# Kernel optimization log

Measured on AMD Instinct MI355X. Metric: run time of the kernel, lower is better.

## Reference

```python
import jax, jax.numpy as jnp
import numpy as np

D_MODEL = 512
D_FF = 4 * D_MODEL
NUM_EXPERTS = 8
TOP_K = 2
NUM_TASKS = 16
D_TASK = 64
BATCH = 8
SEQ = 4096
LN_EPS = 1e-5


def setup_inputs() -> dict:
    key = jax.random.key(0)
    ks = jax.random.split(key, 10)
    s_in = 1.0 / np.sqrt(D_MODEL)
    s_ff = 1.0 / np.sqrt(D_FF)
    s_g = 1.0 / np.sqrt(D_MODEL + D_TASK)
    return {
        "x": jax.random.normal(ks[0], (BATCH, SEQ, D_MODEL), jnp.float32),
        "task_id": jax.random.randint(ks[1], (BATCH,), 0, NUM_TASKS),
        "w1": jax.random.normal(ks[2], (NUM_EXPERTS, D_MODEL, D_FF), jnp.float32) * s_in,
        "b1": jnp.zeros((NUM_EXPERTS, D_FF), jnp.float32),
        "w2": jax.random.normal(ks[3], (NUM_EXPERTS, D_FF, D_MODEL), jnp.float32) * s_ff,
        "b2": jnp.zeros((NUM_EXPERTS, D_MODEL), jnp.float32),
        "task_emb": jax.random.normal(ks[4], (NUM_TASKS, D_TASK), jnp.float32),
        "gate_w": jax.random.normal(ks[5], (D_MODEL + D_TASK, NUM_EXPERTS), jnp.float32) * s_g,
        "gate_b": jnp.zeros((NUM_EXPERTS,), jnp.float32),
    }


def reference(x, task_id, w1, b1, w2, b2, task_emb, gate_w, gate_b):
    B, S, D = x.shape
    E = w1.shape[0]

    # F.layer_norm(x, x.shape[1:]): normalize over (seq, d_model) jointly, no affine
    mean = jnp.mean(x, axis=(1, 2), keepdims=True)
    var = jnp.var(x, axis=(1, 2), keepdims=True)
    x_norm = (x - mean) * jax.lax.rsqrt(var + LN_EPS)

    t_emb = task_emb[task_id]                       # [B, d_task]
    t_emb = jnp.broadcast_to(t_emb[:, None, :], (B, S, t_emb.shape[-1]))
    gate_in = jnp.concatenate([x_norm, t_emb], axis=-1)
    logits = gate_in @ gate_w + gate_b              # [B, S, E]

    topk_logits, topk_idx = jax.lax.top_k(logits, TOP_K)   # [B, S, K]
    topk_probs = jax.nn.softmax(topk_logits, axis=-1)

    flat_x = x.reshape(-1, D)                       # [T, D]
    flat_idx = topk_idx.reshape(-1, TOP_K)          # [T, K]
    flat_p = topk_probs.reshape(-1, TOP_K)          # [T, K]

    assign = jax.nn.one_hot(flat_idx, E, dtype=x.dtype)    # [T, K, E]
    combine = jnp.einsum("tk,tke->te", flat_p, assign)     # [T, E] per-token expert weight

    out = jnp.zeros_like(flat_x)
    for e in range(E):  # fixed small expert loop
        h = jax.nn.silu(flat_x @ w1[e] + b1[e])
        y = h @ w2[e] + b2[e]
        out = out + y * combine[:, e:e + 1]
    final_output = out.reshape(B, S, D)

    usage = jnp.sum(assign, axis=(0, 1))            # [E] assignment counts
    usage_mean = jnp.mean(usage) + 1e-6
    usage_std = jnp.std(usage, ddof=1)              # torch.std is unbiased
    lb_loss = (usage_std / usage_mean) ** 2

    return final_output, lb_loss, topk_idx, task_id
```

## Files before the change

### kernel.cpp

```cpp
#include <hip/hip_runtime.h>

#define NB      8
#define SEQ     4096
#define DM      512
#define DFF     2048
#define NE      8
#define NTOK    32768
#define NPB     2097152
#define MAXROWS 66560
#define MAXTILES 520

#define OUT_LB   16777216
#define OUT_TOPK 16777217
#define OUT_TASK 16842753

#define WS_BSTATS   0
#define WS_DMEAN    8192
#define WS_DRSTD    8256
#define WS_DCOLSUM  8320
#define WS_DTASK    8384
#define WS_HIST     8896
#define WS_CURSOR   8928
#define WS_SEGOFF   8960
#define WS_HDR_END  9216
#define WS_ROUTE_E  9216
#define WS_ROUTE_P  271360
#define WS_ATOK     533504
#define WS_APROB    799744
#define WS_TOKPOS   1065984
#define WS_RAW      1328128
#define WS_W1T      3425280
#define WS_W2T      20202496
#define WS_XB       36979712
#define WS_Y        70534144
#define WS_H        138691584

typedef __attribute__((ext_vector_type(4))) float  f32x4;
typedef __attribute__((ext_vector_type(8))) __bf16 bf16x8;
typedef __attribute__((ext_vector_type(8))) short  s16x8;

__device__ __forceinline__ unsigned short f2bf(float f) {
    unsigned int u = __builtin_bit_cast(unsigned int, f);
    u += 0x7FFFu + ((u >> 16) & 1u);
    return (unsigned short)(u >> 16);
}
__device__ __forceinline__ float bf2f(unsigned short b) {
    unsigned int u = ((unsigned int)b) << 16;
    return __builtin_bit_cast(float, u);
}
__device__ __forceinline__ unsigned int pkbf(float a, float b) {
    unsigned int r;
    asm("v_cvt_pk_bf16_f32 %0, %1, %2" : "=v"(r) : "v"(a), "v"(b));
    return r;
}
__device__ __forceinline__ float silu_f(float v) {
    return v * __builtin_amdgcn_rcpf(1.0f + __expf(-v));
}

#define GLDS16(g, l)                                                              \
    __builtin_amdgcn_global_load_lds(                                             \
        (const __attribute__((address_space(1))) unsigned int*)(const void*)(g),  \
        (__attribute__((address_space(3))) unsigned int*)(void*)(l), 16, 0, 0)

__global__ void k_transpose_bf16(const float* __restrict__ in,
                                 unsigned short* __restrict__ outT,
                                 int R, int C) {
    __shared__ float tile[32][33];
    int e = blockIdx.z;
    const float* src = in + (size_t)e * R * C;
    unsigned short* dst = outT + (size_t)e * R * C;
    int tx = threadIdx.x & 31, ty = threadIdx.x >> 5;
    int c0 = blockIdx.x * 32, r0 = blockIdx.y * 32;
#pragma unroll
    for (int i = 0; i < 4; i++) {
        int r = r0 + ty + i * 8;
        tile[ty + i * 8][tx] = src[(size_t)r * C + c0 + tx];
    }
    __syncthreads();
#pragma unroll
    for (int i = 0; i < 4; i++) {
        int rr = c0 + ty + i * 8;
        dst[(size_t)rr * R + r0 + tx] = f2bf(tile[tx][ty + i * 8]);
    }
}

#define GQPAD 1032
__global__ void __launch_bounds__(256) k_xgate(const float* __restrict__ x,
                                               const float* __restrict__ gw,
                                               unsigned short* __restrict__ xb,
                                               double* __restrict__ bstats,
                                               double* __restrict__ raw) {
    __shared__ float gws[4 * GQPAD];
    int t = threadIdx.x;
#pragma unroll
    for (int i = 0; i < 16; i++) {
        int idx = i * 256 + t;
        int row = idx >> 3, e = idx & 7;
        gws[(row >> 7) * GQPAD + (row & 127) * 8 + e] = gw[idx];
    }
    __syncthreads();

    int token = blockIdx.x * 64 + (t >> 2);
    int q = t & 3;
    const float4* xp = (const float4*)(x + (size_t)token * DM + q * 128);
    unsigned short* xbp = xb + (size_t)token * DM + q * 128;
    const float* gq = &gws[q * GQPAD];

    double acc[8] = {0, 0, 0, 0, 0, 0, 0, 0};
    double s = 0.0, ss = 0.0;
#pragma unroll 4
    for (int i = 0; i < 32; i += 2) {
        float4 v0 = xp[i];
        float4 v1 = xp[i + 1];
        {
            double dx = v0.x, dy = v0.y, dz = v0.z, dw = v0.w;
            const float* g = &gq[i * 32];
#pragma unroll
            for (int e = 0; e < 8; e++)
                acc[e] += dx * (double)g[e] + dy * (double)g[8 + e]
                        + dz * (double)g[16 + e] + dw * (double)g[24 + e];
            s  += dx + dy + dz + dw;
            ss += dx * dx + dy * dy + dz * dz + dw * dw;
        }
        {
            double dx = v1.x, dy = v1.y, dz = v1.z, dw = v1.w;
            const float* g = &gq[(i + 1) * 32];
#pragma unroll
            for (int e = 0; e < 8; e++)
                acc[e] += dx * (double)g[e] + dy * (double)g[8 + e]
                        + dz * (double)g[16 + e] + dw * (double)g[24 + e];
            s  += dx + dy + dz + dw;
            ss += dx * dx + dy * dy + dz * dz + dw * dw;
        }
        s16x8 o = {(short)f2bf(v0.x), (short)f2bf(v0.y), (short)f2bf(v0.z), (short)f2bf(v0.w),
                   (short)f2bf(v1.x), (short)f2bf(v1.y), (short)f2bf(v1.z), (short)f2bf(v1.w)};
        *(s16x8*)(xbp + i * 4) = o;
    }

#pragma unroll
    for (int e = 0; e < 8; e++) {
        acc[e] += __shfl_xor(acc[e], 1);
        acc[e] += __shfl_xor(acc[e], 2);
    }
    if (q == 0) {
#pragma unroll
        for (int e = 0; e < 8; e++) raw[(size_t)token * 8 + e] = acc[e];
    }

    for (int o = 32; o; o >>= 1) { s += __shfl_down(s, o); ss += __shfl_down(ss, o); }
    __shared__ double as_[4], ass_[4];
    int w = t >> 6;
    if ((t & 63) == 0) { as_[w] = s; ass_[w] = ss; }
    __syncthreads();
    if (t == 0) {
        s  = as_[0] + as_[1] + as_[2] + as_[3];
        ss = ass_[0] + ass_[1] + ass_[2] + ass_[3];
        bstats[blockIdx.x * 2]     = s;
        bstats[blockIdx.x * 2 + 1] = ss;
    }
}

__global__ void k_finalize(const double* __restrict__ bstats,
                           double* __restrict__ dmean, double* __restrict__ drstd,
                           double* __restrict__ dcolsum, double* __restrict__ dtask,
                           const float* __restrict__ gw, const float* __restrict__ gb,
                           const float* __restrict__ temb, const int* __restrict__ task_id,
                           float* __restrict__ out_task) {
    int t = threadIdx.x;
    if (t < 8) {
        double s = 0.0, ss = 0.0;
        for (int i = 0; i < 64; i++) {
            s  += bstats[(t * 64 + i) * 2];
            ss += bstats[(t * 64 + i) * 2 + 1];
        }
        double N = (double)NPB;
        double m = s / N;
        double var = ss / N - m * m;
        dmean[t] = m;
        drstd[t] = 1.0 / sqrt(var + 1e-5);
    }
    __shared__ double colp[32][8];
    {
        int e = t & 7, g = t >> 3;
        double a = 0.0;
        for (int r = g * 16; r < g * 16 + 16; r++) a += (double)gw[r * 8 + e];
        colp[g][e] = a;
    }
    __syncthreads();
    if (t < 8) {
        double a = 0.0;
        for (int g = 0; g < 32; g++) a += colp[g][t];
        dcolsum[t] = a;
    }
    if (t < 64) {
        int b2 = t >> 3, e = t & 7;
        int tid = task_id[b2];
        double a = (double)gb[e];
        for (int d = 0; d < 64; d++)
            a += (double)temb[tid * 64 + d] * (double)gw[(512 + d) * 8 + e];
        dtask[t] = a;
    }
    if (t < 8) out_task[t] = (float)task_id[t];
}

__global__ void __launch_bounds__(256) k_topk(const double* __restrict__ raw,
                                              const double* __restrict__ dmean,
                                              const double* __restrict__ drstd,
                                              const double* __restrict__ dcolsum,
                                              const double* __restrict__ dtask,
                                              int* __restrict__ hist,
                                              int2* __restrict__ route_e,
                                              float2* __restrict__ route_p,
                                              float* __restrict__ out_topk) {
    __shared__ int lh[8];
    int t = threadIdx.x;
    if (t < 8) lh[t] = 0;
    __syncthreads();
    int token = blockIdx.x * 256 + t;
    int b = token >> 12;
    double m = dmean[b], rs = drstd[b];
    double lg[8];
#pragma unroll
    for (int e = 0; e < 8; e++)
        lg[e] = rs * (raw[(size_t)token * 8 + e] - m * dcolsum[e]) + dtask[b * 8 + e];
    int i0 = 0;
#pragma unroll
    for (int e = 1; e < 8; e++) if (lg[e] > lg[i0]) i0 = e;
    int i1 = (i0 == 0) ? 1 : 0;
#pragma unroll
    for (int e = 0; e < 8; e++) if (e != i0 && lg[e] > lg[i1]) i1 = e;
    double d = exp(lg[i1] - lg[i0]);
    double p0 = 1.0 / (1.0 + d);
    double p1 = d / (1.0 + d);
    out_topk[token * 2]     = (float)i0;
    out_topk[token * 2 + 1] = (float)i1;
    atomicAdd(&lh[i0], 1);
    atomicAdd(&lh[i1], 1);
    route_e[token] = make_int2(i0, i1);
    route_p[token] = make_float2((float)p0, (float)p1);
    __syncthreads();
    if (t < 8) atomicAdd(&hist[t], lh[t]);
}

__global__ void k_offsets_lb(const int* __restrict__ hist, int* __restrict__ seg_off,
                             float* __restrict__ out_lb) {
    if (threadIdx.x == 0) {
        int off = 0;
        double ssd = 0.0;
        for (int e = 0; e < 8; e++) {
            seg_off[e] = off;
            off += (hist[e] + 127) & ~127;
            double d = (double)hist[e] - 8192.0;
            ssd += d * d;
        }
        seg_off[8] = off;
        double stdv = sqrt(ssd / 7.0);
        double m = 8192.0 + 1e-6;
        double r = stdv / m;
        *out_lb = (float)(r * r);
    }
}

__global__ void __launch_bounds__(256) k_scatter(const int2* __restrict__ route_e,
                                                 const float2* __restrict__ route_p,
                                                 const int* __restrict__ seg_off,
                                                 int* __restrict__ cursor,
                                                 int* __restrict__ atok,
                                                 float* __restrict__ aprob,
                                                 int* __restrict__ tokpos) {
    __shared__ int lcount[8];
    __shared__ int lbase[8];
    int t = threadIdx.x;
    if (t < 8) lcount[t] = 0;
    __syncthreads();
    int tok = blockIdx.x * 256 + t;
    int2 e = route_e[tok];
    float2 p = route_p[tok];
    int p0 = atomicAdd(&lcount[e.x], 1);
    int p1 = atomicAdd(&lcount[e.y], 1);
    __syncthreads();
    if (t < 8) lbase[t] = atomicAdd(&cursor[t], lcount[t]);
    __syncthreads();
    int a0 = seg_off[e.x] + lbase[e.x] + p0;
    atok[a0] = tok; aprob[a0] = p.x;
    int a1 = seg_off[e.y] + lbase[e.y] + p1;
    atok[a1] = tok; aprob[a1] = p.y;
    tokpos[tok * 2]     = a0;
    tokpos[tok * 2 + 1] = a1;
}


__global__ void __launch_bounds__(256) k_gemm1(const unsigned short* __restrict__ xb,
                                               const unsigned short* __restrict__ w1t,
                                               const float* __restrict__ b1,
                                               const int* __restrict__ atok,
                                               const int* __restrict__ seg_off,
                                               unsigned short* __restrict__ H,
                                               int t0) {
    int nwg = (int)gridDim.x;
    int bid = (int)blockIdx.x;
    int wg = (bid & 7) * (nwg >> 3) + (bid >> 3);
    int xt = wg >> 4, y = wg & 15;
    int r0 = (t0 + xt) * 128;
    if (r0 >= seg_off[8]) return;
    int e = 0;
    while (seg_off[e + 1] <= r0) e++;
    int f0 = y * 128;

    int tid = threadIdx.x;
    int w = tid >> 6, l = tid & 63;
    int c = l & 7;

    __shared__ __align__(16) unsigned short As[2][128 * 64];
    __shared__ __align__(16) unsigned short Bs[2][128 * 64];

    const unsigned short* asrc[4];
    const unsigned short* bsrc[4];
    unsigned short*       adst[4];
    unsigned short*       bdst[4];
#pragma unroll
    for (int j = 0; j < 4; j++) {
        int R = w * 32 + j * 8 + (l >> 3);
        int cs = c ^ (R & 7);
        int tok = atok[r0 + R]; if (tok < 0) tok = 0;
        asrc[j] = xb + (size_t)tok * DM + cs * 8;
        bsrc[j] = w1t + ((size_t)e * DFF + f0 + R) * DM + cs * 8;
        adst[j] = &As[0][(size_t)(w * 32 + j * 8) * 64];
        bdst[j] = &Bs[0][(size_t)(w * 32 + j * 8) * 64];
    }

    f32x4 acc[4][4] = {};
    int wr = w >> 1, wc = w & 1, lr = l & 15, q = l >> 4;

#pragma unroll
    for (int j = 0; j < 4; j++) { GLDS16(asrc[j], adst[j]); GLDS16(bsrc[j], bdst[j]); }

    int cur = 0;
    for (int it = 0; it < DM / 64; ++it) {
        if (it + 1 < DM / 64) {
            int kn = (it + 1) * 64;
            int off = (cur ^ 1) * 128 * 64;
#pragma unroll
            for (int j = 0; j < 4; j++) {
                GLDS16(asrc[j] + kn, adst[j] + off);
                GLDS16(bsrc[j] + kn, bdst[j] + off);
            }
            asm volatile("s_waitcnt vmcnt(8)" ::: "memory");
        } else {
            asm volatile("s_waitcnt vmcnt(0)" ::: "memory");
        }
        __builtin_amdgcn_s_barrier();
        __builtin_amdgcn_sched_barrier(0);
        __builtin_amdgcn_s_setprio(1);
        const unsigned short* Ab = &As[cur][0];
        const unsigned short* Bb = &Bs[cur][0];
#pragma unroll
        for (int h = 0; h < 2; h++) {
            bf16x8 af[4], bfv[4];
#pragma unroll
            for (int m = 0; m < 4; m++) {
                int R = wr * 64 + m * 16 + lr;
                af[m] = *(const bf16x8*)&Ab[R * 64 + (((h << 2) + q) ^ (R & 7)) * 8];
            }
#pragma unroll
            for (int n = 0; n < 4; n++) {
                int R = wc * 64 + n * 16 + lr;
                bfv[n] = *(const bf16x8*)&Bb[R * 64 + (((h << 2) + q) ^ (R & 7)) * 8];
            }
#pragma unroll
            for (int m = 0; m < 4; m++)
#pragma unroll
                for (int n = 0; n < 4; n++)
                    acc[m][n] = __builtin_amdgcn_mfma_f32_16x16x32_bf16(bfv[n], af[m], acc[m][n], 0, 0, 0);
        }
        __builtin_amdgcn_s_setprio(0);
        __builtin_amdgcn_sched_barrier(0);
        asm volatile("" ::: "memory");
        __builtin_amdgcn_s_barrier();
        cur ^= 1;
    }

    const float* b1e = b1 + e * DFF + f0;
#pragma unroll
    for (int m = 0; m < 4; m++) {
        int r = wr * 64 + m * 16 + lr;
        unsigned short* hrow = H + ((size_t)xt * 128 + r) * DFF + f0;
#pragma unroll
        for (int n = 0; n < 4; n++) {
            int fc = wc * 64 + n * 16 + q * 4;
            float4 bias = *(const float4*)(b1e + fc);
            float v0 = silu_f(acc[m][n][0] + bias.x);
            float v1 = silu_f(acc[m][n][1] + bias.y);
            float v2 = silu_f(acc[m][n][2] + bias.z);
            float v3 = silu_f(acc[m][n][3] + bias.w);
            *(uint2*)(hrow + fc) = make_uint2(pkbf(v0, v1), pkbf(v2, v3));
        }
    }
}

__global__ void __launch_bounds__(256) k_gemm2(const unsigned short* __restrict__ H,
                                               const unsigned short* __restrict__ w2t,
                                               const int* __restrict__ seg_off,
                                               unsigned short* __restrict__ Y,
                                               int t0) {
    int nwg = (int)gridDim.x;
    int bid = (int)blockIdx.x;
    int wg = (bid & 7) * (nwg >> 3) + (bid >> 3);
    int xt = wg >> 2, y = wg & 3;
    int r0 = (t0 + xt) * 128;
    if (r0 >= seg_off[8]) return;
    int e = 0;
    while (seg_off[e + 1] <= r0) e++;
    int d0 = y * 128;

    int tid = threadIdx.x;
    int w = tid >> 6, l = tid & 63;
    int c = l & 7;

    __shared__ __align__(16) unsigned short As[2][128 * 64];
    __shared__ __align__(16) unsigned short Bs[2][128 * 64];

    const unsigned short* asrc[4];
    const unsigned short* bsrc[4];
    unsigned short*       adst[4];
    unsigned short*       bdst[4];
#pragma unroll
    for (int j = 0; j < 4; j++) {
        int R = w * 32 + j * 8 + (l >> 3);
        int cs = c ^ (R & 7);
        asrc[j] = H + ((size_t)xt * 128 + R) * DFF + cs * 8;
        bsrc[j] = w2t + ((size_t)e * DM + d0 + R) * DFF + cs * 8;
        adst[j] = &As[0][(size_t)(w * 32 + j * 8) * 64];
        bdst[j] = &Bs[0][(size_t)(w * 32 + j * 8) * 64];
    }

    f32x4 acc[4][4] = {};
    int wr = w >> 1, wc = w & 1, lr = l & 15, q = l >> 4;

#pragma unroll
    for (int j = 0; j < 4; j++) { GLDS16(asrc[j], adst[j]); GLDS16(bsrc[j], bdst[j]); }

    int cur = 0;
    for (int it = 0; it < DFF / 64; ++it) {
        if (it + 1 < DFF / 64) {
            int kn = (it + 1) * 64;
            int off = (cur ^ 1) * 128 * 64;
#pragma unroll
            for (int j = 0; j < 4; j++) {
                GLDS16(asrc[j] + kn, adst[j] + off);
                GLDS16(bsrc[j] + kn, bdst[j] + off);
            }
            asm volatile("s_waitcnt vmcnt(8)" ::: "memory");
        } else {
            asm volatile("s_waitcnt vmcnt(0)" ::: "memory");
        }
        __builtin_amdgcn_s_barrier();
        __builtin_amdgcn_sched_barrier(0);
        __builtin_amdgcn_s_setprio(1);
        const unsigned short* Ab = &As[cur][0];
        const unsigned short* Bb = &Bs[cur][0];
#pragma unroll
        for (int h = 0; h < 2; h++) {
            bf16x8 af[4], bfv[4];
#pragma unroll
            for (int m = 0; m < 4; m++) {
                int R = wr * 64 + m * 16 + lr;
                af[m] = *(const bf16x8*)&Ab[R * 64 + (((h << 2) + q) ^ (R & 7)) * 8];
            }
#pragma unroll
            for (int n = 0; n < 4; n++) {
                int R = wc * 64 + n * 16 + lr;
                bfv[n] = *(const bf16x8*)&Bb[R * 64 + (((h << 2) + q) ^ (R & 7)) * 8];
            }
#pragma unroll
            for (int m = 0; m < 4; m++)
#pragma unroll
                for (int n = 0; n < 4; n++)
                    acc[m][n] = __builtin_amdgcn_mfma_f32_16x16x32_bf16(bfv[n], af[m], acc[m][n], 0, 0, 0);
        }
        __builtin_amdgcn_s_setprio(0);
        __builtin_amdgcn_sched_barrier(0);
        asm volatile("" ::: "memory");
        __builtin_amdgcn_s_barrier();
        cur ^= 1;
    }

#pragma unroll
    for (int m = 0; m < 4; m++) {
        int r = wr * 64 + m * 16 + lr;
        unsigned short* yrow = Y + (size_t)(r0 + r) * DM + d0;
#pragma unroll
        for (int n = 0; n < 4; n++) {
            int dc = wc * 64 + n * 16 + q * 4;
            *(uint2*)(yrow + dc) = make_uint2(pkbf(acc[m][n][0], acc[m][n][1]),
                                              pkbf(acc[m][n][2], acc[m][n][3]));
        }
    }
}

__global__ void __launch_bounds__(256) k_combine(const unsigned short* __restrict__ Y,
                                                 const float* __restrict__ b2,
                                                 const int* __restrict__ tokpos,
                                                 const int2* __restrict__ route_e,
                                                 const float2* __restrict__ route_p,
                                                 float* __restrict__ out) {
    int gt = blockIdx.x * 256 + threadIdx.x;
    int token = gt >> 6;
    int cbase = (gt & 63) * 8;
    int2 e = route_e[token];
    float2 p = route_p[token];
    int a0 = tokpos[token * 2], a1 = tokpos[token * 2 + 1];
    s16x8 y0 = *(const s16x8*)(Y + (size_t)a0 * DM + cbase);
    s16x8 y1 = *(const s16x8*)(Y + (size_t)a1 * DM + cbase);
    const float4* bb0 = (const float4*)(b2 + e.x * DM + cbase);
    const float4* bb1 = (const float4*)(b2 + e.y * DM + cbase);
    float4 b00 = bb0[0], b01 = bb0[1];
    float4 b10 = bb1[0], b11 = bb1[1];
    float r[8];
    r[0] = p.x * (bf2f((unsigned short)y0[0]) + b00.x) + p.y * (bf2f((unsigned short)y1[0]) + b10.x);
    r[1] = p.x * (bf2f((unsigned short)y0[1]) + b00.y) + p.y * (bf2f((unsigned short)y1[1]) + b10.y);
    r[2] = p.x * (bf2f((unsigned short)y0[2]) + b00.z) + p.y * (bf2f((unsigned short)y1[2]) + b10.z);
    r[3] = p.x * (bf2f((unsigned short)y0[3]) + b00.w) + p.y * (bf2f((unsigned short)y1[3]) + b10.w);
    r[4] = p.x * (bf2f((unsigned short)y0[4]) + b01.x) + p.y * (bf2f((unsigned short)y1[4]) + b11.x);
    r[5] = p.x * (bf2f((unsigned short)y0[5]) + b01.y) + p.y * (bf2f((unsigned short)y1[5]) + b11.y);
    r[6] = p.x * (bf2f((unsigned short)y0[6]) + b01.z) + p.y * (bf2f((unsigned short)y1[6]) + b11.z);
    r[7] = p.x * (bf2f((unsigned short)y0[7]) + b01.w) + p.y * (bf2f((unsigned short)y1[7]) + b11.w);
    float* op = out + (size_t)token * DM + cbase;
    *(float4*)op       = make_float4(r[0], r[1], r[2], r[3]);
    *(float4*)(op + 4) = make_float4(r[4], r[5], r[6], r[7]);
}

extern "C" void kernel_launch(void* const* d_in, const int* in_sizes, int n_in,
                              void* d_out, int out_size, void* d_ws, size_t ws_size,
                              hipStream_t stream) {
    const float* x       = (const float*)d_in[0];
    const int*   task_id = (const int*)d_in[1];
    const float* w1      = (const float*)d_in[2];
    const float* b1      = (const float*)d_in[3];
    const float* w2      = (const float*)d_in[4];
    const float* b2      = (const float*)d_in[5];
    const float* temb    = (const float*)d_in[6];
    const float* gw      = (const float*)d_in[7];
    const float* gb      = (const float*)d_in[8];
    float* out = (float*)d_out;

    char* ws = (char*)d_ws;
    double* bstats   = (double*)(ws + WS_BSTATS);
    double* dmean    = (double*)(ws + WS_DMEAN);
    double* drstd    = (double*)(ws + WS_DRSTD);
    double* dcolsum  = (double*)(ws + WS_DCOLSUM);
    double* dtask    = (double*)(ws + WS_DTASK);
    int*    hist     = (int*)(ws + WS_HIST);
    int*    cursor   = (int*)(ws + WS_CURSOR);
    int*    seg_off  = (int*)(ws + WS_SEGOFF);
    int2*   route_e  = (int2*)(ws + WS_ROUTE_E);
    float2* route_p  = (float2*)(ws + WS_ROUTE_P);
    int*    atok     = (int*)(ws + WS_ATOK);
    float*  aprob    = (float*)(ws + WS_APROB);
    int*    tokpos   = (int*)(ws + WS_TOKPOS);
    double* raw      = (double*)(ws + WS_RAW);
    unsigned short* w1t = (unsigned short*)(ws + WS_W1T);
    unsigned short* w2t = (unsigned short*)(ws + WS_W2T);
    unsigned short* xb  = (unsigned short*)(ws + WS_XB);
    unsigned short* Y   = (unsigned short*)(ws + WS_Y);
    unsigned short* H   = (unsigned short*)(ws + WS_H);

    int TPC = (int)((ws_size - (size_t)WS_H) / (size_t)(128 * DFF * 2));
    if (TPC > 128) TPC = 128;
    TPC &= ~1;
    if (TPC < 2) TPC = 2;

    hipMemsetAsync(ws, 0, WS_HDR_END, stream);
    hipMemsetAsync(ws + WS_ATOK, 0xFF, (size_t)MAXROWS * sizeof(int), stream);

    k_transpose_bf16<<<dim3(DFF / 32, DM / 32, NE), 256, 0, stream>>>(w1, w1t, DM, DFF);
    k_transpose_bf16<<<dim3(DM / 32, DFF / 32, NE), 256, 0, stream>>>(w2, w2t, DFF, DM);

    k_xgate<<<NTOK / 64, 256, 0, stream>>>(x, gw, xb, bstats, raw);
    k_finalize<<<1, 256, 0, stream>>>(bstats, dmean, drstd, dcolsum, dtask,
                                      gw, gb, temb, task_id, out + OUT_TASK);
    k_topk<<<NTOK / 256, 256, 0, stream>>>(raw, dmean, drstd, dcolsum, dtask,
                                           hist, route_e, route_p, out + OUT_TOPK);
    k_offsets_lb<<<1, 64, 0, stream>>>(hist, seg_off, out + OUT_LB);
    k_scatter<<<NTOK / 256, 256, 0, stream>>>(route_e, route_p, seg_off, cursor,
                                              atok, aprob, tokpos);

    for (int t0 = 0; t0 < MAXTILES; t0 += TPC) {
        k_gemm1<<<TPC * 16, 256, 0, stream>>>(xb, w1t, b1, atok, seg_off, H, t0);
        k_gemm2<<<TPC * 4, 256, 0, stream>>>(H, w2t, seg_off, Y, t0);
    }
    k_combine<<<NTOK / 4, 256, 0, stream>>>(Y, b2, tokpos, route_e, route_p, out);
}
```

Baseline: 549.1 us.

## Simplify gemm1 to single-buffered BK=32 tiles and merge final chunk tail

Replaces the double-buffered, XOR-swizzled BK=64 LDS pipeline in the first expert GEMM with a single-buffered BK=32 loop that loads, syncs, computes and syncs again each step. This shrinks LDS use, which could allow more resident workgroups, but it gives up the overlap of global loads with MFMA work and brings back LDS bank conflicts from the unswizzled layout. The host loop also changes how tiles are split into chunks so that a small leftover is folded into the last launch, cutting one gemm1/gemm2 launch pair.

```diff
diff --git a/kernel.cpp b/kernel.cpp
--- a/kernel.cpp
+++ b/kernel.cpp
@@ -289,7 +289,6 @@
     tokpos[tok * 2 + 1] = a1;
 }
 
-
 __global__ void __launch_bounds__(256) k_gemm1(const unsigned short* __restrict__ xb,
                                                const unsigned short* __restrict__ w1t,
                                                const float* __restrict__ b1,
@@ -309,75 +308,48 @@
 
     int tid = threadIdx.x;
     int w = tid >> 6, l = tid & 63;
-    int c = l & 7;
-
-    __shared__ __align__(16) unsigned short As[2][128 * 64];
-    __shared__ __align__(16) unsigned short Bs[2][128 * 64];
-
-    const unsigned short* asrc[4];
-    const unsigned short* bsrc[4];
-    unsigned short*       adst[4];
-    unsigned short*       bdst[4];
-#pragma unroll
-    for (int j = 0; j < 4; j++) {
-        int R = w * 32 + j * 8 + (l >> 3);
-        int cs = c ^ (R & 7);
-        int tok = atok[r0 + R]; if (tok < 0) tok = 0;
-        asrc[j] = xb + (size_t)tok * DM + cs * 8;
-        bsrc[j] = w1t + ((size_t)e * DFF + f0 + R) * DM + cs * 8;
-        adst[j] = &As[0][(size_t)(w * 32 + j * 8) * 64];
-        bdst[j] = &Bs[0][(size_t)(w * 32 + j * 8) * 64];
-    }
+    int wr = w >> 1, wc = w & 1, lr = l & 15, q = l >> 4;
+
+    __shared__ __align__(16) unsigned short As[128 * 32];
+    __shared__ __align__(16) unsigned short Bs[128 * 32];
+
+    int rsub = l >> 2;
+    int koff = (l & 3) * 8;
+    int row0 = w * 16 + rsub;
+    int row1 = row0 + 64;
+    int tok0 = atok[r0 + row0]; if (tok0 < 0) tok0 = 0;
+    int tok1 = atok[r0 + row1]; if (tok1 < 0) tok1 = 0;
+    const unsigned short* a0 = xb + (size_t)tok0 * DM + koff;
+    const unsigned short* a1 = xb + (size_t)tok1 * DM + koff;
+    const unsigned short* b0 = w1t + ((size_t)e * DFF + f0 + row0) * DM + koff;
+    const unsigned short* b1p = w1t + ((size_t)e * DFF + f0 + row1) * DM + koff;
+    unsigned short* ad0 = &As[(w * 16) * 32];
+    unsigned short* ad1 = &As[(w * 16 + 64) * 32];
+    unsigned short* bd0 = &Bs[(w * 16) * 32];
+    unsigned short* bd1 = &Bs[(w * 16 + 64) * 32];
 
     f32x4 acc[4][4] = {};
-    int wr = w >> 1, wc = w & 1, lr = l & 15, q = l >> 4;
-
-#pragma unroll
-    for (int j = 0; j < 4; j++) { GLDS16(asrc[j], adst[j]); GLDS16(bsrc[j], bdst[j]); }
-
-    int cur = 0;
-    for (int it = 0; it < DM / 64; ++it) {
-        if (it + 1 < DM / 64) {
-            int kn = (it + 1) * 64;
-            int off = (cur ^ 1) * 128 * 64;
-#pragma unroll
-            for (int j = 0; j < 4; j++) {
-                GLDS16(asrc[j] + kn, adst[j] + off);
-                GLDS16(bsrc[j] + kn, bdst[j] + off);
-            }
-            asm volatile("s_waitcnt vmcnt(8)" ::: "memory");
-        } else {
-            asm volatile("s_waitcnt vmcnt(0)" ::: "memory");
-        }
-        __builtin_amdgcn_s_barrier();
-        __builtin_amdgcn_sched_barrier(0);
-        __builtin_amdgcn_s_setprio(1);
-        const unsigned short* Ab = &As[cur][0];
-        const unsigned short* Bb = &Bs[cur][0];
-#pragma unroll
-        for (int h = 0; h < 2; h++) {
-            bf16x8 af[4], bfv[4];
-#pragma unroll
-            for (int m = 0; m < 4; m++) {
-                int R = wr * 64 + m * 16 + lr;
-                af[m] = *(const bf16x8*)&Ab[R * 64 + (((h << 2) + q) ^ (R & 7)) * 8];
-            }
-#pragma unroll
-            for (int n = 0; n < 4; n++) {
-                int R = wc * 64 + n * 16 + lr;
-                bfv[n] = *(const bf16x8*)&Bb[R * 64 + (((h << 2) + q) ^ (R & 7)) * 8];
-            }
-#pragma unroll
-            for (int m = 0; m < 4; m++)
-#pragma unroll
-                for (int n = 0; n < 4; n++)
-                    acc[m][n] = __builtin_amdgcn_mfma_f32_16x16x32_bf16(bfv[n], af[m], acc[m][n], 0, 0, 0);
-        }
-        __builtin_amdgcn_s_setprio(0);
-        __builtin_amdgcn_sched_barrier(0);
-        asm volatile("" ::: "memory");
-        __builtin_amdgcn_s_barrier();
-        cur ^= 1;
+
+    for (int kt = 0; kt < DM / 32; ++kt) {
+        int kk = kt * 32;
+        GLDS16(a0 + kk, ad0);
+        GLDS16(a1 + kk, ad1);
+        GLDS16(b0 + kk, bd0);
+        GLDS16(b1p + kk, bd1);
+        __syncthreads();
+        bf16x8 af[4], bfv[4];
+#pragma unroll
+        for (int m = 0; m < 4; m++)
+            af[m] = *(const bf16x8*)&As[(wr * 64 + m * 16 + lr) * 32 + q * 8];
+#pragma unroll
+        for (int n = 0; n < 4; n++)
+            bfv[n] = *(const bf16x8*)&Bs[(wc * 64 + n * 16 + lr) * 32 + q * 8];
+#pragma unroll
+        for (int m = 0; m < 4; m++)
+#pragma unroll
+            for (int n = 0; n < 4; n++)
+                acc[m][n] = __builtin_amdgcn_mfma_f32_16x16x32_bf16(bfv[n], af[m], acc[m][n], 0, 0, 0);
+        __syncthreads();
     }
 
     const float* b1e = b1 + e * DFF + f0;
@@ -565,7 +537,8 @@
     unsigned short* Y   = (unsigned short*)(ws + WS_Y);
     unsigned short* H   = (unsigned short*)(ws + WS_H);
 
-    int TPC = (int)((ws_size - (size_t)WS_H) / (size_t)(128 * DFF * 2));
+    int space_tiles = (int)((ws_size - (size_t)WS_H) / (size_t)(128 * DFF * 2));
+    int TPC = space_tiles;
     if (TPC > 128) TPC = 128;
     TPC &= ~1;
     if (TPC < 2) TPC = 2;
@@ -585,9 +558,17 @@
     k_scatter<<<NTOK / 256, 256, 0, stream>>>(route_e, route_p, seg_off, cursor,
                                               atok, aprob, tokpos);
 
-    for (int t0 = 0; t0 < MAXTILES; t0 += TPC) {
-        k_gemm1<<<TPC * 16, 256, 0, stream>>>(xb, w1t, b1, atok, seg_off, H, t0);
-        k_gemm2<<<TPC * 4, 256, 0, stream>>>(H, w2t, seg_off, Y, t0);
+    int t0 = 0;
+    while (t0 < MAXTILES) {
+        int rem = MAXTILES - t0;
+        int tpc_c = TPC;
+        if (rem > TPC && rem <= TPC + 16 && rem <= space_tiles) tpc_c = rem;
+        else if (rem <= TPC) tpc_c = rem;
+        tpc_c &= ~1;
+        if (tpc_c < 2) tpc_c = 2;
+        k_gemm1<<<tpc_c * 16, 256, 0, stream>>>(xb, w1t, b1, atok, seg_off, H, t0);
+        k_gemm2<<<tpc_c * 4, 256, 0, stream>>>(H, w2t, seg_off, Y, t0);
+        t0 += tpc_c;
     }
     k_combine<<<NTOK / 4, 256, 0, stream>>>(Y, b2, tokpos, route_e, route_p, out);
 }
```

Result: slower. 566.4 us (+3.2%).
